# Kernel tuning notes

Measured on AMD Instinct MI355X. Metric: run time of the kernel, lower is better.

The kernel has to match this reference:

```python
import jax, jax.numpy as jnp
import numpy as np

P, B, I, O = 32, 512, 1024, 1024


def setup_inputs() -> dict:
    key = jax.random.key(0)
    kx, kw = jax.random.split(key)
    # strictly {0,1}-valued binary tensors stored as float32, as in the torch module
    x = (jax.random.uniform(kx, (P, B, I)) > 0.5).astype(jnp.float32)
    w = (jax.random.uniform(kw, (2, P, I, O)) > 0.5).astype(jnp.float32)
    return {"x": x, "w": w}


def reference(x, w):
    # x: [P, B, I] binary; w: [2, P, I, O] binary.
    # out = x @ W0 + (~x) @ W1  (logical_not of a {0,1} float is 1 - x)
    notx = 1.0 - x
    out = jnp.einsum('pbi,pio->pbo', x, w[0]) + jnp.einsum('pbi,pio->pbo', notx, w[1])
    return out  # [P, B, O], activation == 'none'
```

## Files before the change

### kernel.cpp

```cpp
#include <hip/hip_runtime.h>


namespace {

constexpr int PP = 32;
constexpr int BB = 512;
constexpr int II = 1024;
constexpr int OO = 1024;

constexpr int BM = 256;
constexpr int BN = 128;
constexpr int BK = 32;

constexpr int KPA = 40;

__device__ __forceinline__ int boff(int o, int k) {
    return o * 40 + (o >> 2) * 8 + k;
}

typedef __attribute__((ext_vector_type(8))) short bf16x8;
typedef __attribute__((ext_vector_type(4))) float f32x4;

constexpr int A_BYTES = BM * KPA * 2;
constexpr int B_BYTES = (BN * 40 + (BN / 4) * 8) * 2;
constexpr int SMEM_BYTES = A_BYTES + B_BYTES;

__device__ __forceinline__ unsigned pk2(float lo, float hi) {
    return (__float_as_uint(lo) >> 16) | (__float_as_uint(hi) & 0xFFFF0000u);
}

__global__ __launch_bounds__(512, 4) void ebl_kernel(const float* __restrict__ x,
                                                     const float* __restrict__ w,
                                                     float* __restrict__ out) {
    __shared__ __align__(16) char smem[SMEM_BYTES];
    unsigned short* As = (unsigned short*)smem;
    unsigned short* Bs = (unsigned short*)(smem + A_BYTES);
    float* Scr    = (float*)smem;
    float* ColSum = (float*)(smem + 8192);

    const int t  = (int)threadIdx.x;
    const int l  = t & 63;
    const int wv = t >> 6;
    const int wm = wv & 3;
    const int wn = wv >> 2;
    const int lq = l >> 4;
    const int ln = l & 15;

    const int bid = (int)blockIdx.x;
    const int wid = (bid & 7) * 64 + (bid >> 3);
    const int p   = wid >> 4;
    const int rem = wid & 15;
    const int b0  = (rem & 1) * BM;
    const int o0  = (rem >> 1) * BN;

    const float* xp  = x + ((size_t)p * BB + b0) * II;
    const float* w0p = w + (size_t)p * II * OO;
    const float* w1p = w + (size_t)(PP + p) * II * OO;

    const int a_row = t >> 3;
    const int a_col = (t & 7) * 4;
    const int bk0 = 2 * (t >> 5);
    const int og  = (t & 31) * 4;

    int a_rd[4], b_rd[4];
#pragma unroll
    for (int mt = 0; mt < 4; ++mt)
        a_rd[mt] = (wm * 64 + mt * 16 + ln) * KPA + lq * 8;
#pragma unroll
    for (int nt = 0; nt < 4; ++nt)
        b_rd[nt] = boff(wn * 64 + nt * 16 + ln, lq * 8);

    f32x4 acc[4][4];
#pragma unroll
    for (int mt = 0; mt < 4; ++mt)
#pragma unroll
        for (int nt = 0; nt < 4; ++nt)
            acc[mt][nt] = (f32x4){0.f, 0.f, 0.f, 0.f};

    f32x4 csum = (f32x4){0.f, 0.f, 0.f, 0.f};

    const float* xa0  = xp + (size_t)a_row * II + a_col;
    const float* xa1  = xa0 + (size_t)64 * II;
    const float* xa2  = xa0 + (size_t)128 * II;
    const float* xa3  = xa0 + (size_t)192 * II;
    const float* wb00 = w0p + (size_t)bk0 * OO + o0 + og;
    const float* wb01 = wb00 + OO;
    const float* wb10 = w1p + (size_t)bk0 * OO + o0 + og;
    const float* wb11 = wb10 + OO;

    for (int kk = 0; kk < II; kk += BK) {
        f32x4 a0  = *(const f32x4*)(xa0 + kk);
        f32x4 a1  = *(const f32x4*)(xa1 + kk);
        f32x4 a2  = *(const f32x4*)(xa2 + kk);
        f32x4 a3  = *(const f32x4*)(xa3 + kk);
        f32x4 q00 = *(const f32x4*)(wb00 + (size_t)kk * OO);
        f32x4 q01 = *(const f32x4*)(wb01 + (size_t)kk * OO);
        f32x4 q10 = *(const f32x4*)(wb10 + (size_t)kk * OO);
        f32x4 q11 = *(const f32x4*)(wb11 + (size_t)kk * OO);

        __syncthreads();

        *(uint2*)(&As[a_row * KPA + a_col]) =
            make_uint2(pk2(a0.x, a0.y), pk2(a0.z, a0.w));
        *(uint2*)(&As[(a_row + 64) * KPA + a_col]) =
            make_uint2(pk2(a1.x, a1.y), pk2(a1.z, a1.w));
        *(uint2*)(&As[(a_row + 128) * KPA + a_col]) =
            make_uint2(pk2(a2.x, a2.y), pk2(a2.z, a2.w));
        *(uint2*)(&As[(a_row + 192) * KPA + a_col]) =
            make_uint2(pk2(a3.x, a3.y), pk2(a3.z, a3.w));

        f32x4 d0 = q00 - q10;
        f32x4 d1 = q01 - q11;
        csum += q10;
        csum += q11;
#pragma unroll
        for (int c = 0; c < 4; ++c)
            *(unsigned*)(&Bs[boff(og + c, bk0)]) = pk2(d0[c], d1[c]);

        __syncthreads();

        bf16x8 af[4], bfm[4];
#pragma unroll
        for (int mt = 0; mt < 4; ++mt)
            af[mt] = *(const bf16x8*)(&As[a_rd[mt]]);
#pragma unroll
        for (int nt = 0; nt < 4; ++nt)
            bfm[nt] = *(const bf16x8*)(&Bs[b_rd[nt]]);
#pragma unroll
        for (int mt = 0; mt < 4; ++mt)
#pragma unroll
            for (int nt = 0; nt < 4; ++nt)
                acc[mt][nt] = __builtin_amdgcn_mfma_f32_16x16x32_bf16(
                    af[mt], bfm[nt], acc[mt][nt], 0, 0, 0);
    }

    __syncthreads();
    *(f32x4*)(&Scr[(t >> 5) * 128 + og]) = csum;
    __syncthreads();
    if (t < 128) {
        float s = 0.f;
#pragma unroll
        for (int q = 0; q < 16; ++q) s += Scr[q * 128 + t];
        ColSum[t] = s;
    }
    __syncthreads();

    float* op = out + (size_t)p * BB * OO + o0;
#pragma unroll
    for (int nt = 0; nt < 4; ++nt) {
        const int ocol = wn * 64 + nt * 16 + ln;
        const float cs = ColSum[ocol];
#pragma unroll
        for (int mt = 0; mt < 4; ++mt) {
            const int row = b0 + wm * 64 + mt * 16 + lq * 4;
#pragma unroll
            for (int r = 0; r < 4; ++r)
                op[(size_t)(row + r) * OO + ocol] = acc[mt][nt][r] + cs;
        }
    }
}

}

extern "C" void kernel_launch(void* const* d_in, const int* in_sizes, int n_in,
                              void* d_out, int out_size, void* d_ws, size_t ws_size,
                              hipStream_t stream) {
    const float* x = (const float*)d_in[0];
    const float* w = (const float*)d_in[1];
    float* out = (float*)d_out;
    dim3 grid(PP * (BB / BM) * (OO / BN), 1, 1);
    ebl_kernel<<<grid, dim3(512, 1, 1), 0, stream>>>(x, w, out);
}
```

Measured before the change: 432.3 us.

## Halve M tile and double-buffer LDS with register prefetch of next K slice

Shrinks the block tile from 256x128 to 128x128 and remaps the 8 waves to a 2x4 layout, which doubles the grid and halves per-wave accumulators. Adds a second LDS buffer so only one barrier per K step is needed, and issues the global loads for the next K slice right after the barrier so they overlap the MFMA work. The trade-off is that each W tile is re-read by twice as many blocks, roughly doubling W global traffic, in exchange for more parallelism and better latency hiding.

```diff
diff --git a/kernel.cpp b/kernel.cpp
--- a/kernel.cpp
+++ b/kernel.cpp
@@ -8,7 +8,7 @@
 constexpr int II = 1024;
 constexpr int OO = 1024;
 
-constexpr int BM = 256;
+constexpr int BM = 128;
 constexpr int BN = 128;
 constexpr int BK = 32;
 
@@ -23,7 +23,8 @@
 
 constexpr int A_BYTES = BM * KPA * 2;
 constexpr int B_BYTES = (BN * 40 + (BN / 4) * 8) * 2;
-constexpr int SMEM_BYTES = A_BYTES + B_BYTES;
+constexpr int BUF_BYTES = A_BYTES + B_BYTES;
+constexpr int SMEM_BYTES = 2 * BUF_BYTES;
 
 __device__ __forceinline__ unsigned pk2(float lo, float hi) {
     return (__float_as_uint(lo) >> 16) | (__float_as_uint(hi) & 0xFFFF0000u);
@@ -33,25 +34,23 @@
                                                      const float* __restrict__ w,
                                                      float* __restrict__ out) {
     __shared__ __align__(16) char smem[SMEM_BYTES];
-    unsigned short* As = (unsigned short*)smem;
-    unsigned short* Bs = (unsigned short*)(smem + A_BYTES);
     float* Scr    = (float*)smem;
     float* ColSum = (float*)(smem + 8192);
 
     const int t  = (int)threadIdx.x;
     const int l  = t & 63;
     const int wv = t >> 6;
-    const int wm = wv & 3;
-    const int wn = wv >> 2;
+    const int wm = wv & 1;
+    const int wn = wv >> 1;
     const int lq = l >> 4;
     const int ln = l & 15;
 
     const int bid = (int)blockIdx.x;
-    const int wid = (bid & 7) * 64 + (bid >> 3);
-    const int p   = wid >> 4;
-    const int rem = wid & 15;
-    const int b0  = (rem & 1) * BM;
-    const int o0  = (rem >> 1) * BN;
+    const int wid = (bid & 7) * 128 + (bid >> 3);
+    const int p   = wid >> 5;
+    const int rem = wid & 31;
+    const int b0  = (rem & 3) * BM;
+    const int o0  = (rem >> 2) * BN;
 
     const float* xp  = x + ((size_t)p * BB + b0) * II;
     const float* w0p = w + (size_t)p * II * OO;
@@ -62,53 +61,46 @@
     const int bk0 = 2 * (t >> 5);
     const int og  = (t & 31) * 4;
 
-    int a_rd[4], b_rd[4];
+    int a_rd[4], b_rd[2];
 #pragma unroll
     for (int mt = 0; mt < 4; ++mt)
         a_rd[mt] = (wm * 64 + mt * 16 + ln) * KPA + lq * 8;
 #pragma unroll
-    for (int nt = 0; nt < 4; ++nt)
-        b_rd[nt] = boff(wn * 64 + nt * 16 + ln, lq * 8);
+    for (int nt = 0; nt < 2; ++nt)
+        b_rd[nt] = boff(wn * 32 + nt * 16 + ln, lq * 8);
 
-    f32x4 acc[4][4];
+    f32x4 acc[4][2];
 #pragma unroll
     for (int mt = 0; mt < 4; ++mt)
 #pragma unroll
-        for (int nt = 0; nt < 4; ++nt)
+        for (int nt = 0; nt < 2; ++nt)
             acc[mt][nt] = (f32x4){0.f, 0.f, 0.f, 0.f};
 
     f32x4 csum = (f32x4){0.f, 0.f, 0.f, 0.f};
 
     const float* xa0  = xp + (size_t)a_row * II + a_col;
     const float* xa1  = xa0 + (size_t)64 * II;
-    const float* xa2  = xa0 + (size_t)128 * II;
-    const float* xa3  = xa0 + (size_t)192 * II;
     const float* wb00 = w0p + (size_t)bk0 * OO + o0 + og;
     const float* wb01 = wb00 + OO;
     const float* wb10 = w1p + (size_t)bk0 * OO + o0 + og;
     const float* wb11 = wb10 + OO;
 
+    f32x4 a0  = *(const f32x4*)(xa0);
+    f32x4 a1  = *(const f32x4*)(xa1);
+    f32x4 q00 = *(const f32x4*)(wb00);
+    f32x4 q01 = *(const f32x4*)(wb01);
+    f32x4 q10 = *(const f32x4*)(wb10);
+    f32x4 q11 = *(const f32x4*)(wb11);
+
     for (int kk = 0; kk < II; kk += BK) {
-        f32x4 a0  = *(const f32x4*)(xa0 + kk);
-        f32x4 a1  = *(const f32x4*)(xa1 + kk);
-        f32x4 a2  = *(const f32x4*)(xa2 + kk);
-        f32x4 a3  = *(const f32x4*)(xa3 + kk);
-        f32x4 q00 = *(const f32x4*)(wb00 + (size_t)kk * OO);
-        f32x4 q01 = *(const f32x4*)(wb01 + (size_t)kk * OO);
-        f32x4 q10 = *(const f32x4*)(wb10 + (size_t)kk * OO);
-        f32x4 q11 = *(const f32x4*)(wb11 + (size_t)kk * OO);
-
-        __syncthreads();
+        char* buf = smem + ((kk >> 5) & 1) * BUF_BYTES;
+        unsigned short* As = (unsigned short*)buf;
+        unsigned short* Bs = (unsigned short*)(buf + A_BYTES);
 
         *(uint2*)(&As[a_row * KPA + a_col]) =
             make_uint2(pk2(a0.x, a0.y), pk2(a0.z, a0.w));
         *(uint2*)(&As[(a_row + 64) * KPA + a_col]) =
             make_uint2(pk2(a1.x, a1.y), pk2(a1.z, a1.w));
-        *(uint2*)(&As[(a_row + 128) * KPA + a_col]) =
-            make_uint2(pk2(a2.x, a2.y), pk2(a2.z, a2.w));
-        *(uint2*)(&As[(a_row + 192) * KPA + a_col]) =
-            make_uint2(pk2(a3.x, a3.y), pk2(a3.z, a3.w));
-
         f32x4 d0 = q00 - q10;
         f32x4 d1 = q01 - q11;
         csum += q10;
@@ -119,19 +111,28 @@
 
         __syncthreads();
 
-        bf16x8 af[4], bfm[4];
+        const int kn = kk + BK;
+        if (kn < II) {
+            a0  = *(const f32x4*)(xa0 + kn);
+            a1  = *(const f32x4*)(xa1 + kn);
+            q00 = *(const f32x4*)(wb00 + (size_t)kn * OO);
+            q01 = *(const f32x4*)(wb01 + (size_t)kn * OO);
+            q10 = *(const f32x4*)(wb10 + (size_t)kn * OO);
+            q11 = *(const f32x4*)(wb11 + (size_t)kn * OO);
+        }
+
+        bf16x8 bfm[2];
 #pragma unroll
-        for (int mt = 0; mt < 4; ++mt)
-            af[mt] = *(const bf16x8*)(&As[a_rd[mt]]);
-#pragma unroll
-        for (int nt = 0; nt < 4; ++nt)
+        for (int nt = 0; nt < 2; ++nt)
             bfm[nt] = *(const bf16x8*)(&Bs[b_rd[nt]]);
 #pragma unroll
-        for (int mt = 0; mt < 4; ++mt)
+        for (int mt = 0; mt < 4; ++mt) {
+            bf16x8 af = *(const bf16x8*)(&As[a_rd[mt]]);
 #pragma unroll
-            for (int nt = 0; nt < 4; ++nt)
+            for (int nt = 0; nt < 2; ++nt)
                 acc[mt][nt] = __builtin_amdgcn_mfma_f32_16x16x32_bf16(
-                    af[mt], bfm[nt], acc[mt][nt], 0, 0, 0);
+                    af, bfm[nt], acc[mt][nt], 0, 0, 0);
+        }
     }
 
     __syncthreads();
@@ -147,8 +148,8 @@
 
     float* op = out + (size_t)p * BB * OO + o0;
 #pragma unroll
-    for (int nt = 0; nt < 4; ++nt) {
-        const int ocol = wn * 64 + nt * 16 + ln;
+    for (int nt = 0; nt < 2; ++nt) {
+        const int ocol = wn * 32 + nt * 16 + ln;
         const float cs = ColSum[ocol];
 #pragma unroll
         for (int mt = 0; mt < 4; ++mt) {
```

Measured after the change: 439.8 us. About the same (+1.7%).
